# Kernel tuning notes

Hardware: AMD Instinct MI355X
Metric: run time of the kernel (lower is better)

## Reference

```python
import jax, jax.numpy as jnp
import numpy as np

D_K = 64  # d_model=512 // n_heads=8, hardcoded in source
NEG = -1e9


def setup_inputs() -> dict:
    key = jax.random.key(0)
    kq, kk, kv, km = jax.random.split(key, 4)
    B, H, S, D = 2, 8, 2048, D_K
    Q = jax.random.normal(kq, (B, H, S, D), dtype=jnp.float32)
    K = jax.random.normal(kk, (B, H, S, D), dtype=jnp.float32)
    V = jax.random.normal(kv, (B, H, S, D), dtype=jnp.float32)
    attn_mask = jax.random.randint(km, (B, H, S, S), 0, 2).astype(jnp.bool_)
    return {"Q": Q, "K": K, "V": V, "attn_mask": attn_mask}


def reference(Q, K, V, attn_mask):
    # scores = Q @ (K^T / sqrt(d_k))  -- scale applied to K^T as in source
    scale = 1.0 / np.sqrt(D_K).astype(np.float32)
    scores = jnp.einsum('bhqd,bhkd->bhqk', Q, K * scale)
    scores = jnp.where(attn_mask, NEG, scores)
    attn = jax.nn.softmax(scores, axis=-1)
    context = jnp.einsum('bhqk,bhkd->bhqd', attn, V)
    return (context, attn)
```

## Files before the change

### kernel.cpp

```cpp
#include <hip/hip_runtime.h>

typedef float f32x4 __attribute__((ext_vector_type(4)));
typedef _Float16 f16x4 __attribute__((ext_vector_type(4)));
typedef unsigned int u32x4 __attribute__((ext_vector_type(4)));
typedef __bf16 bf16x8_t __attribute__((ext_vector_type(8)));
typedef __bf16 bf16x4_t __attribute__((ext_vector_type(4)));

#define DEVFN static __device__ __forceinline__

constexpr int BHN = 16;
constexpr int SN  = 2048;
constexpr int DN  = 64;
constexpr size_t CTXN = (size_t)BHN * SN * DN;
constexpr int NK1 = 4;
constexpr int NK2 = 4;

DEVFN void qk4_mfma(f32x4& dA, f32x4& dB, bf16x8_t k0v, bf16x8_t k1v,
                    bf16x8_t qA0, bf16x8_t qA1, bf16x8_t qB0, bf16x8_t qB1) {
  asm volatile("s_nop 3\n\t"
               "v_mfma_f32_16x16x32_bf16 %0, %2, %4, %0\n\t"
               "v_mfma_f32_16x16x32_bf16 %1, %2, %6, %1\n\t"
               "v_mfma_f32_16x16x32_bf16 %0, %3, %5, %0\n\t"
               "v_mfma_f32_16x16x32_bf16 %1, %3, %7, %1\n\t"
               "s_nop 7\n\ts_nop 7"
               : "+v"(dA), "+v"(dB)
               : "v"(k0v), "v"(k1v), "v"(qA0), "v"(qA1), "v"(qB0), "v"(qB1));
}

DEVFN void pv8_mfma(f32x4& a0, f32x4& a1, f32x4& a2, f32x4& a3,
                    f32x4& b0, f32x4& b1, f32x4& b2, f32x4& b3,
                    bf16x4_t paA, bf16x4_t paB,
                    bf16x4_t v0, bf16x4_t v1, bf16x4_t v2, bf16x4_t v3) {
  asm volatile("s_nop 3\n\t"
               "v_mfma_f32_16x16x16_bf16 %0, %8, %10, %0\n\t"
               "v_mfma_f32_16x16x16_bf16 %4, %9, %10, %4\n\t"
               "v_mfma_f32_16x16x16_bf16 %1, %8, %11, %1\n\t"
               "v_mfma_f32_16x16x16_bf16 %5, %9, %11, %5\n\t"
               "v_mfma_f32_16x16x16_bf16 %2, %8, %12, %2\n\t"
               "v_mfma_f32_16x16x16_bf16 %6, %9, %12, %6\n\t"
               "v_mfma_f32_16x16x16_bf16 %3, %8, %13, %3\n\t"
               "v_mfma_f32_16x16x16_bf16 %7, %9, %13, %7\n\t"
               "s_nop 7\n\ts_nop 7"
               : "+v"(a0), "+v"(a1), "+v"(a2), "+v"(a3),
                 "+v"(b0), "+v"(b1), "+v"(b2), "+v"(b3)
               : "v"(paA), "v"(paB), "v"(v0), "v"(v1), "v"(v2), "v"(v3));
}

__global__ __launch_bounds__(256) void pack_mask_T_kernel(
    const void* __restrict__ mraw, unsigned int* __restrict__ bmT) {
  __shared__ unsigned int sfl;
  if (threadIdx.x == 0) sfl = 0;
  __syncthreads();
  {
    unsigned int f = 0;
    const unsigned int* m32 = (const unsigned int*)mraw;
    for (int i = threadIdx.x; i < 4096; i += 256) {
      unsigned int w = m32[i];
      if (w == 0x3F800000u) f |= 2u;
      else if (w > 1u) f |= 1u;
    }
    if (f) atomicOr(&sfl, f);
  }
  __syncthreads();
  const unsigned int fl = (sfl & 2u) ? 2u : ((sfl & 1u) ? 1u : 0u);

  const int tid = blockIdx.x * 256 + threadIdx.x;
  const int NT  = gridDim.x * 256;
  if (fl != 1u) {
    const int W = BHN * (SN / 32) * SN;
    const unsigned int* m32 = (const unsigned int*)mraw;
    for (int w = tid; w < W; w += NT) {
      const int q   = w & (SN - 1);
      const int kc2 = (w >> 11) & (SN / 32 - 1);
      const int bh  = w >> 17;
      const unsigned int* src = m32 + ((size_t)(bh * SN + q) * SN) + kc2 * 32;
      unsigned int r = 0;
      #pragma unroll
      for (int j = 0; j < 8; ++j) {
        u32x4 v = *(const u32x4*)(src + j * 4);
        r |= ((unsigned)(v[0] != 0u)) << (4 * j)
           | ((unsigned)(v[1] != 0u)) << (4 * j + 1)
           | ((unsigned)(v[2] != 0u)) << (4 * j + 2)
           | ((unsigned)(v[3] != 0u)) << (4 * j + 3);
      }
      bmT[w] = r;
    }
  } else {
    const int W4 = BHN * (SN / 128) * SN;
    const unsigned char* m8 = (const unsigned char*)mraw;
    for (int w4 = tid; w4 < W4; w4 += NT) {
      const int q   = w4 & (SN - 1);
      const int kc8 = (w4 >> 11) & (SN / 128 - 1);
      const int bh  = w4 >> 15;
      const unsigned char* src = m8 + ((size_t)(bh * SN + q) * SN) + kc8 * 128;
      #pragma unroll
      for (int i = 0; i < 4; ++i) {
        const unsigned int* s32 = (const unsigned int*)(src + 32 * i);
        unsigned int r = 0;
        #pragma unroll
        for (int j = 0; j < 8; ++j) {
          unsigned int x = s32[j];
          r |= ((unsigned)((x & 0x000000FFu) != 0u)) << (4 * j)
             | ((unsigned)((x & 0x0000FF00u) != 0u)) << (4 * j + 1)
             | ((unsigned)((x & 0x00FF0000u) != 0u)) << (4 * j + 2)
             | ((unsigned)((x & 0xFF000000u) != 0u)) << (4 * j + 3);
        }
        bmT[((size_t)(bh * (SN / 32) + kc8 * 4 + i)) * SN + q] = r;
      }
    }
  }
}

__global__ __launch_bounds__(256) void conv_qk_kernel(
    const float* __restrict__ Q, const float* __restrict__ K,
    __bf16* __restrict__ Qb, __bf16* __restrict__ Kb) {
  const size_t i = ((size_t)blockIdx.x * 256 + threadIdx.x) * 4;
  const float* src = blockIdx.y ? K : Q;
  __bf16* dst = blockIdx.y ? Kb : Qb;
  const float scale = blockIdx.y ? 0.125f : 1.0f;
  f32x4 v = *(const f32x4*)(src + i);
  bf16x4_t o = {(__bf16)(v[0] * scale), (__bf16)(v[1] * scale),
                (__bf16)(v[2] * scale), (__bf16)(v[3] * scale)};
  *(bf16x4_t*)(dst + i) = o;
}

__global__ __launch_bounds__(256) void conv_vt_kernel(
    const float* __restrict__ V, __bf16* __restrict__ Vt) {
  const int lane = threadIdx.x & 63, wv = threadIdx.x >> 6;
  const int k0 = (blockIdx.x * 4 + wv) * 32;
  const int bh = blockIdx.y;
  const float* src = V + (size_t)bh * SN * DN;
  __bf16* dst = Vt + (((size_t)bh * (SN / 32) + (k0 >> 5)) * DN + lane) * 32;
  bf16x8_t w0, w1, w2, w3;
  #pragma unroll
  for (int i = 0; i < 8; ++i) {
    w0[i] = (__bf16)src[(size_t)(k0 + i) * DN + lane];
    w1[i] = (__bf16)src[(size_t)(k0 + 8 + i) * DN + lane];
    w2[i] = (__bf16)src[(size_t)(k0 + 16 + i) * DN + lane];
    w3[i] = (__bf16)src[(size_t)(k0 + 24 + i) * DN + lane];
  }
  *(bf16x8_t*)(dst)      = w0;
  *(bf16x8_t*)(dst + 8)  = w1;
  *(bf16x8_t*)(dst + 16) = w2;
  *(bf16x8_t*)(dst + 24) = w3;
}

DEVFN void swz_decode(int bid, int& bh, int& c, int& x) {
  const int xcd = bid & 7, s8 = bid >> 3;
  bh = xcd + 8 * (s8 >> 6);
  const int r6 = s8 & 63;
  c = r6 >> 4;
  x = r6 & 15;
}

__global__ __launch_bounds__(256, 4) void attn_l_kernel(
    const __bf16* __restrict__ Qb, const __bf16* __restrict__ Kb,
    const unsigned int* __restrict__ bmT, float* __restrict__ lpart) {
  const int lane = threadIdx.x & 63, wv = threadIdx.x >> 6;
  const int qr = lane & 15, g = lane >> 4;
  int bh, c, x;
  swz_decode(blockIdx.x, bh, c, x);
  const int q0 = x * 128 + wv * 32;
  const int CS = SN / NK1, kbeg = c * CS;
  const __bf16* Qbb = Qb + (size_t)bh * SN * DN;
  const __bf16* Kbb = Kb + (size_t)bh * SN * DN;
  const int qA = q0 + qr, qB = q0 + 16 + qr;
  bf16x8_t qfA0 = *(const bf16x8_t*)(Qbb + (size_t)qA * DN + 8 * g);
  bf16x8_t qfA1 = *(const bf16x8_t*)(Qbb + (size_t)qA * DN + 32 + 8 * g);
  bf16x8_t qfB0 = *(const bf16x8_t*)(Qbb + (size_t)qB * DN + 8 * g);
  bf16x8_t qfB1 = *(const bf16x8_t*)(Qbb + (size_t)qB * DN + 32 + 8 * g);
  const size_t rowA = (size_t)bh * SN + qA;
  const size_t rowB = (size_t)bh * SN + qB;
  const unsigned int* bmb = bmT + (size_t)bh * (SN / 32) * SN;

  bf16x8_t kf0 = *(const bf16x8_t*)(Kbb + (size_t)(kbeg + qr) * DN + 8 * g);
  bf16x8_t kf1 = *(const bf16x8_t*)(Kbb + (size_t)(kbeg + qr) * DN + 32 + 8 * g);
  float lA = 0.f, lB = 0.f;
  unsigned int wmA = 0, wmB = 0;
  #pragma unroll 2
  for (int t = 0; t < CS / 16; ++t) {
    const int kt = kbeg + t * 16;
    const int kn = kbeg + ((t + 1) & (CS / 16 - 1)) * 16;
    bf16x8_t nk0 = *(const bf16x8_t*)(Kbb + (size_t)(kn + qr) * DN + 8 * g);
    bf16x8_t nk1 = *(const bf16x8_t*)(Kbb + (size_t)(kn + qr) * DN + 32 + 8 * g);
    if ((t & 1) == 0) {
      wmA = bmb[(size_t)(kt >> 5) * SN + qA];
      wmB = bmb[(size_t)(kt >> 5) * SN + qB];
    }
    f32x4 aA = {0,0,0,0}, aB = {0,0,0,0};
    qk4_mfma(aA, aB, kf0, kf1, qfA0, qfA1, qfB0, qfB1);
    const int sh = (kt & 16) + 4 * g;
    lA += ((wmA >> (sh + 0)) & 1u) ? 0.f : __expf(aA[0]);
    lA += ((wmA >> (sh + 1)) & 1u) ? 0.f : __expf(aA[1]);
    lA += ((wmA >> (sh + 2)) & 1u) ? 0.f : __expf(aA[2]);
    lA += ((wmA >> (sh + 3)) & 1u) ? 0.f : __expf(aA[3]);
    lB += ((wmB >> (sh + 0)) & 1u) ? 0.f : __expf(aB[0]);
    lB += ((wmB >> (sh + 1)) & 1u) ? 0.f : __expf(aB[1]);
    lB += ((wmB >> (sh + 2)) & 1u) ? 0.f : __expf(aB[2]);
    lB += ((wmB >> (sh + 3)) & 1u) ? 0.f : __expf(aB[3]);
    kf0 = nk0; kf1 = nk1;
  }
  lA = lA + __shfl_xor(lA, 16); lA = lA + __shfl_xor(lA, 32);
  lB = lB + __shfl_xor(lB, 16); lB = lB + __shfl_xor(lB, 32);
  if (g == 0) {
    lpart[rowA * NK1 + c] = lA;
    lpart[rowB * NK1 + c] = lB;
  }
}

__global__ __launch_bounds__(256, 4) void attn_out_kernel(
    const __bf16* __restrict__ Qb, const __bf16* __restrict__ Kb,
    const __bf16* __restrict__ Vt, const unsigned int* __restrict__ bmT,
    const float* __restrict__ lpart, _Float16* __restrict__ cp,
    float* __restrict__ attn) {
  __shared__ __align__(16) char Ks[2][4096];
  __shared__ __align__(16) char Vs[2][4096];
  const int tid = threadIdx.x;
  const int lane = tid & 63, wv = tid >> 6;
  const int qr = lane & 15, g = lane >> 4;
  int bh, c, x;
  swz_decode(blockIdx.x, bh, c, x);
  const int q0 = x * 128 + wv * 32;
  const int CS = SN / NK2, kbase = c * CS;
  const int NT = CS / 32;

  const __bf16* Qbb = Qb + (size_t)bh * SN * DN;
  const int qA = q0 + qr, qB = q0 + 16 + qr;
  bf16x8_t qfA0 = *(const bf16x8_t*)(Qbb + (size_t)qA * DN + 8 * g);
  bf16x8_t qfA1 = *(const bf16x8_t*)(Qbb + (size_t)qA * DN + 32 + 8 * g);
  bf16x8_t qfB0 = *(const bf16x8_t*)(Qbb + (size_t)qB * DN + 8 * g);
  bf16x8_t qfB1 = *(const bf16x8_t*)(Qbb + (size_t)qB * DN + 32 + 8 * g);
  const size_t rowA = (size_t)bh * SN + qA;
  const size_t rowB = (size_t)bh * SN + qB;
  f32x4 l4A = *(const f32x4*)(lpart + rowA * NK1);
  f32x4 l4B = *(const f32x4*)(lpart + rowB * NK1);
  const float rlA = 1.0f / (l4A[0] + l4A[1] + l4A[2] + l4A[3]);
  const float rlB = 1.0f / (l4B[0] + l4B[1] + l4B[2] + l4B[3]);
  const unsigned int* bmb = bmT + (size_t)bh * (SN / 32) * SN;
  float* arowA = attn + rowA * SN;
  float* arowB = attn + rowB * SN;

  const int krow = tid >> 3;
  const int kcolb = (tid & 7) * 16;
  const int kdst = krow * 128 + (kcolb ^ ((krow & 7) << 4));
  const char* Ksrc = (const char*)(Kb + (size_t)bh * SN * DN + (size_t)kbase * DN);
  const int vd = tid >> 2;
  const int vkb = (tid & 3) * 16;
  const int vdst0 = vd * 64 + ((vkb    ) ^ ((vd & 7) << 3));
  const int vdst1 = vd * 64 + ((vkb + 8) ^ ((vd & 7) << 3));
  const char* Vsrc = (const char*)Vt + ((size_t)bh * (SN / 32) + (kbase >> 5)) * 4096;

  f32x4 cA0 = {0,0,0,0}, cA1 = {0,0,0,0}, cA2 = {0,0,0,0}, cA3 = {0,0,0,0};
  f32x4 cB0 = {0,0,0,0}, cB1 = {0,0,0,0}, cB2 = {0,0,0,0}, cB3 = {0,0,0,0};

  {
    u32x4 kr = *(const u32x4*)(Ksrc + krow * 128 + kcolb);
    u32x4 vr = *(const u32x4*)(Vsrc + tid * 16);
    *(u32x4*)&Ks[0][kdst] = kr;
    *(unsigned long long*)&Vs[0][vdst0] =
        ((unsigned long long)vr[1] << 32) | vr[0];
    *(unsigned long long*)&Vs[0][vdst1] =
        ((unsigned long long)vr[3] << 32) | vr[2];
  }
  __syncthreads();

  for (int tt = 0; tt < NT; ++tt) {
    const bool pf = (tt + 1 < NT);
    u32x4 kr, vr;
    if (pf) {
      kr = *(const u32x4*)(Ksrc + (tt + 1) * 4096 + krow * 128 + kcolb);
      vr = *(const u32x4*)(Vsrc + (tt + 1) * 4096 + tid * 16);
    }
    const char* Kbuf = Ks[tt & 1];
    const char* Vbuf = Vs[tt & 1];
    const int ktg = kbase + tt * 32;
    const unsigned int wmA = bmb[(size_t)((kbase >> 5) + tt) * SN + qA];
    const unsigned int wmB = bmb[(size_t)((kbase >> 5) + tt) * SN + qB];
    #pragma unroll
    for (int s = 0; s < 2; ++s) {
      const int rk = 16 * s + qr;
      bf16x8_t kf0 = *(const bf16x8_t*)&Kbuf[rk * 128 + ((16 * g     ) ^ ((rk & 7) << 4))];
      bf16x8_t kf1 = *(const bf16x8_t*)&Kbuf[rk * 128 + ((64 + 16 * g) ^ ((rk & 7) << 4))];
      const int vxor = (32 * s + 8 * g) ^ ((qr & 7) << 3);
      bf16x4_t vf0 = *(const bf16x4_t*)&Vbuf[(qr     ) * 64 + vxor];
      bf16x4_t vf1 = *(const bf16x4_t*)&Vbuf[(qr + 16) * 64 + vxor];
      bf16x4_t vf2 = *(const bf16x4_t*)&Vbuf[(qr + 32) * 64 + vxor];
      bf16x4_t vf3 = *(const bf16x4_t*)&Vbuf[(qr + 48) * 64 + vxor];
      f32x4 aA = {0,0,0,0}, aB = {0,0,0,0};
      qk4_mfma(aA, aB, kf0, kf1, qfA0, qfA1, qfB0, qfB1);
      const int sh = 16 * s + 4 * g;
      float pA0 = (((wmA >> (sh + 0)) & 1u) ? 0.f : __expf(aA[0])) * rlA;
      float pA1 = (((wmA >> (sh + 1)) & 1u) ? 0.f : __expf(aA[1])) * rlA;
      float pA2 = (((wmA >> (sh + 2)) & 1u) ? 0.f : __expf(aA[2])) * rlA;
      float pA3 = (((wmA >> (sh + 3)) & 1u) ? 0.f : __expf(aA[3])) * rlA;
      float pB0 = (((wmB >> (sh + 0)) & 1u) ? 0.f : __expf(aB[0])) * rlB;
      float pB1 = (((wmB >> (sh + 1)) & 1u) ? 0.f : __expf(aB[1])) * rlB;
      float pB2 = (((wmB >> (sh + 2)) & 1u) ? 0.f : __expf(aB[2])) * rlB;
      float pB3 = (((wmB >> (sh + 3)) & 1u) ? 0.f : __expf(aB[3])) * rlB;
      *(f32x4*)(arowA + ktg + sh) = (f32x4){pA0, pA1, pA2, pA3};
      *(f32x4*)(arowB + ktg + sh) = (f32x4){pB0, pB1, pB2, pB3};
      bf16x4_t paA = {(__bf16)pA0, (__bf16)pA1, (__bf16)pA2, (__bf16)pA3};
      bf16x4_t paB = {(__bf16)pB0, (__bf16)pB1, (__bf16)pB2, (__bf16)pB3};
      pv8_mfma(cA0, cA1, cA2, cA3, cB0, cB1, cB2, cB3, paA, paB, vf0, vf1, vf2, vf3);
    }
    if (pf) {
      char* Kn = Ks[(tt + 1) & 1];
      char* Vn = Vs[(tt + 1) & 1];
      *(u32x4*)&Kn[kdst] = kr;
      *(unsigned long long*)&Vn[vdst0] = ((unsigned long long)vr[1] << 32) | vr[0];
      *(unsigned long long*)&Vn[vdst1] = ((unsigned long long)vr[3] << 32) | vr[2];
    }
    __syncthreads();
  }
  _Float16* cdst = cp + (size_t)c * CTXN;
  const size_t baseo = (size_t)bh * SN * DN;
  #pragma unroll
  for (int j = 0; j < 4; ++j) {
    const size_t rA = baseo + (size_t)(q0 + 4 * g + j) * DN + qr;
    const size_t rB = baseo + (size_t)(q0 + 16 + 4 * g + j) * DN + qr;
    cdst[rA]      = (_Float16)cA0[j];
    cdst[rA + 16] = (_Float16)cA1[j];
    cdst[rA + 32] = (_Float16)cA2[j];
    cdst[rA + 48] = (_Float16)cA3[j];
    cdst[rB]      = (_Float16)cB0[j];
    cdst[rB + 16] = (_Float16)cB1[j];
    cdst[rB + 32] = (_Float16)cB2[j];
    cdst[rB + 48] = (_Float16)cB3[j];
  }
}

__global__ __launch_bounds__(256) void ctx_reduce_kernel(
    const _Float16* __restrict__ cp, float* __restrict__ ctx) {
  const size_t i = ((size_t)blockIdx.x * 256 + threadIdx.x) * 4;
  f16x4 a = *(const f16x4*)(cp + i);
  f16x4 b = *(const f16x4*)(cp + CTXN + i);
  f16x4 d = *(const f16x4*)(cp + 2 * CTXN + i);
  f16x4 e = *(const f16x4*)(cp + 3 * CTXN + i);
  f32x4 s;
  #pragma unroll
  for (int k = 0; k < 4; ++k)
    s[k] = ((float)a[k] + (float)b[k]) + ((float)d[k] + (float)e[k]);
  __builtin_nontemporal_store(s, (f32x4*)(ctx + i));
}

extern "C" void kernel_launch(void* const* d_in, const int* in_sizes, int n_in,
                              void* d_out, int out_size, void* d_ws, size_t ws_size,
                              hipStream_t stream) {
  const float* Q = (const float*)d_in[0];
  const float* K = (const float*)d_in[1];
  const float* V = (const float*)d_in[2];
  const void*  mraw = d_in[3];

  float* out  = (float*)d_out;
  float* ctx  = out;
  float* attn = out + CTXN;

  char* wsb = (char*)d_ws;
  unsigned int* bmT = (unsigned int*)(wsb + 256);
  float* lp   = (float*)(wsb + 256 + 8388608);
  __bf16* Qb  = (__bf16*)(wsb + 256 + 8388608 + 524288);
  __bf16* Kb  = (__bf16*)(wsb + 256 + 8388608 + 524288 + 4194304);
  __bf16* Vt  = (__bf16*)(wsb + 256 + 8388608 + 524288 + 2 * 4194304);
  _Float16* cp = (_Float16*)(wsb + 256 + 8388608 + 524288 + 3 * 4194304);

  pack_mask_T_kernel<<<2048, 256, 0, stream>>>(mraw, bmT);
  conv_qk_kernel<<<dim3(2048, 2), 256, 0, stream>>>(Q, K, Qb, Kb);
  conv_vt_kernel<<<dim3(16, BHN), 256, 0, stream>>>(V, Vt);

  attn_l_kernel<<<1024, 256, 0, stream>>>(Qb, Kb, bmT, lp);
  attn_out_kernel<<<1024, 256, 0, stream>>>(Qb, Kb, Vt, bmT, lp, cp, attn);
  ctx_reduce_kernel<<<2048, 256, 0, stream>>>(cp, ctx);
}
```

Before: 232.8 us.

## Merge prep kernels into one launch and stage K tiles through LDS in attn_l

The three preprocessing kernels (mask bit-pack, Q/K bf16 conversion, V transpose) are combined into a single launch that dispatches on block index, and the Q/K conversion now handles 8 elements per thread. attn_l_kernel now loads 64-row K tiles cooperatively into double-buffered, XOR-swizzled shared memory, with a register prefetch of the next tile, instead of having each wave read K directly from global memory. This aims to cut launch overhead and redundant global K traffic across the four waves. In exchange it adds a block barrier per tile and uses more LDS, which may lower occupancy.

```diff
diff --git a/kernel.cpp b/kernel.cpp
--- a/kernel.cpp
+++ b/kernel.cpp
@@ -46,103 +46,111 @@
                : "v"(paA), "v"(paB), "v"(v0), "v"(v1), "v"(v2), "v"(v3));
 }
 
-__global__ __launch_bounds__(256) void pack_mask_T_kernel(
-    const void* __restrict__ mraw, unsigned int* __restrict__ bmT) {
-  __shared__ unsigned int sfl;
-  if (threadIdx.x == 0) sfl = 0;
-  __syncthreads();
-  {
-    unsigned int f = 0;
-    const unsigned int* m32 = (const unsigned int*)mraw;
-    for (int i = threadIdx.x; i < 4096; i += 256) {
-      unsigned int w = m32[i];
-      if (w == 0x3F800000u) f |= 2u;
-      else if (w > 1u) f |= 1u;
-    }
-    if (f) atomicOr(&sfl, f);
-  }
-  __syncthreads();
-  const unsigned int fl = (sfl & 2u) ? 2u : ((sfl & 1u) ? 1u : 0u);
-
-  const int tid = blockIdx.x * 256 + threadIdx.x;
-  const int NT  = gridDim.x * 256;
-  if (fl != 1u) {
-    const int W = BHN * (SN / 32) * SN;
-    const unsigned int* m32 = (const unsigned int*)mraw;
-    for (int w = tid; w < W; w += NT) {
-      const int q   = w & (SN - 1);
-      const int kc2 = (w >> 11) & (SN / 32 - 1);
-      const int bh  = w >> 17;
-      const unsigned int* src = m32 + ((size_t)(bh * SN + q) * SN) + kc2 * 32;
-      unsigned int r = 0;
-      #pragma unroll
-      for (int j = 0; j < 8; ++j) {
-        u32x4 v = *(const u32x4*)(src + j * 4);
-        r |= ((unsigned)(v[0] != 0u)) << (4 * j)
-           | ((unsigned)(v[1] != 0u)) << (4 * j + 1)
-           | ((unsigned)(v[2] != 0u)) << (4 * j + 2)
-           | ((unsigned)(v[3] != 0u)) << (4 * j + 3);
+constexpr int PB = 2048, QB = 1024, KB = 1024, VB = 256;
+
+__global__ __launch_bounds__(256) void prep_kernel(
+    const void* __restrict__ mraw, unsigned int* __restrict__ bmT,
+    const float* __restrict__ Q, const float* __restrict__ K,
+    const float* __restrict__ V, __bf16* __restrict__ Qb,
+    __bf16* __restrict__ Kb, __bf16* __restrict__ Vt) {
+  const int bid = blockIdx.x;
+  const int tidl = threadIdx.x;
+  if (bid < PB) {
+    __shared__ unsigned int sfl;
+    if (tidl == 0) sfl = 0;
+    __syncthreads();
+    {
+      unsigned int f = 0;
+      const unsigned int* m32 = (const unsigned int*)mraw;
+      for (int i = tidl; i < 4096; i += 256) {
+        unsigned int w = m32[i];
+        if (w == 0x3F800000u) f |= 2u;
+        else if (w > 1u) f |= 1u;
       }
-      bmT[w] = r;
-    }
-  } else {
-    const int W4 = BHN * (SN / 128) * SN;
-    const unsigned char* m8 = (const unsigned char*)mraw;
-    for (int w4 = tid; w4 < W4; w4 += NT) {
-      const int q   = w4 & (SN - 1);
-      const int kc8 = (w4 >> 11) & (SN / 128 - 1);
-      const int bh  = w4 >> 15;
-      const unsigned char* src = m8 + ((size_t)(bh * SN + q) * SN) + kc8 * 128;
-      #pragma unroll
-      for (int i = 0; i < 4; ++i) {
-        const unsigned int* s32 = (const unsigned int*)(src + 32 * i);
+      if (f) atomicOr(&sfl, f);
+    }
+    __syncthreads();
+    const unsigned int fl = (sfl & 2u) ? 2u : ((sfl & 1u) ? 1u : 0u);
+    const int tid = bid * 256 + tidl;
+    const int NT  = PB * 256;
+    if (fl != 1u) {
+      const int W = BHN * (SN / 32) * SN;
+      const unsigned int* m32 = (const unsigned int*)mraw;
+      for (int w = tid; w < W; w += NT) {
+        const int q   = w & (SN - 1);
+        const int kc2 = (w >> 11) & (SN / 32 - 1);
+        const int bh  = w >> 17;
+        const unsigned int* src = m32 + ((size_t)(bh * SN + q) * SN) + kc2 * 32;
         unsigned int r = 0;
         #pragma unroll
         for (int j = 0; j < 8; ++j) {
-          unsigned int x = s32[j];
-          r |= ((unsigned)((x & 0x000000FFu) != 0u)) << (4 * j)
-             | ((unsigned)((x & 0x0000FF00u) != 0u)) << (4 * j + 1)
-             | ((unsigned)((x & 0x00FF0000u) != 0u)) << (4 * j + 2)
-             | ((unsigned)((x & 0xFF000000u) != 0u)) << (4 * j + 3);
+          u32x4 v = *(const u32x4*)(src + j * 4);
+          r |= ((unsigned)(v[0] != 0u)) << (4 * j)
+             | ((unsigned)(v[1] != 0u)) << (4 * j + 1)
+             | ((unsigned)(v[2] != 0u)) << (4 * j + 2)
+             | ((unsigned)(v[3] != 0u)) << (4 * j + 3);
         }
-        bmT[((size_t)(bh * (SN / 32) + kc8 * 4 + i)) * SN + q] = r;
+        bmT[w] = r;
       }
-    }
-  }
-}
-
-__global__ __launch_bounds__(256) void conv_qk_kernel(
-    const float* __restrict__ Q, const float* __restrict__ K,
-    __bf16* __restrict__ Qb, __bf16* __restrict__ Kb) {
-  const size_t i = ((size_t)blockIdx.x * 256 + threadIdx.x) * 4;
-  const float* src = blockIdx.y ? K : Q;
-  __bf16* dst = blockIdx.y ? Kb : Qb;
-  const float scale = blockIdx.y ? 0.125f : 1.0f;
-  f32x4 v = *(const f32x4*)(src + i);
-  bf16x4_t o = {(__bf16)(v[0] * scale), (__bf16)(v[1] * scale),
-                (__bf16)(v[2] * scale), (__bf16)(v[3] * scale)};
-  *(bf16x4_t*)(dst + i) = o;
-}
-
-__global__ __launch_bounds__(256) void conv_vt_kernel(
-    const float* __restrict__ V, __bf16* __restrict__ Vt) {
-  const int lane = threadIdx.x & 63, wv = threadIdx.x >> 6;
-  const int k0 = (blockIdx.x * 4 + wv) * 32;
-  const int bh = blockIdx.y;
-  const float* src = V + (size_t)bh * SN * DN;
-  __bf16* dst = Vt + (((size_t)bh * (SN / 32) + (k0 >> 5)) * DN + lane) * 32;
-  bf16x8_t w0, w1, w2, w3;
-  #pragma unroll
-  for (int i = 0; i < 8; ++i) {
-    w0[i] = (__bf16)src[(size_t)(k0 + i) * DN + lane];
-    w1[i] = (__bf16)src[(size_t)(k0 + 8 + i) * DN + lane];
-    w2[i] = (__bf16)src[(size_t)(k0 + 16 + i) * DN + lane];
-    w3[i] = (__bf16)src[(size_t)(k0 + 24 + i) * DN + lane];
-  }
-  *(bf16x8_t*)(dst)      = w0;
-  *(bf16x8_t*)(dst + 8)  = w1;
-  *(bf16x8_t*)(dst + 16) = w2;
-  *(bf16x8_t*)(dst + 24) = w3;
+    } else {
+      const int W4 = BHN * (SN / 128) * SN;
+      const unsigned char* m8 = (const unsigned char*)mraw;
+      for (int w4 = tid; w4 < W4; w4 += NT) {
+        const int q   = w4 & (SN - 1);
+        const int kc8 = (w4 >> 11) & (SN / 128 - 1);
+        const int bh  = w4 >> 15;
+        const unsigned char* src = m8 + ((size_t)(bh * SN + q) * SN) + kc8 * 128;
+        #pragma unroll
+        for (int i = 0; i < 4; ++i) {
+          const unsigned int* s32 = (const unsigned int*)(src + 32 * i);
+          unsigned int r = 0;
+          #pragma unroll
+          for (int j = 0; j < 8; ++j) {
+            unsigned int x = s32[j];
+            r |= ((unsigned)((x & 0x000000FFu) != 0u)) << (4 * j)
+               | ((unsigned)((x & 0x0000FF00u) != 0u)) << (4 * j + 1)
+               | ((unsigned)((x & 0x00FF0000u) != 0u)) << (4 * j + 2)
+               | ((unsigned)((x & 0xFF000000u) != 0u)) << (4 * j + 3);
+          }
+          bmT[((size_t)(bh * (SN / 32) + kc8 * 4 + i)) * SN + q] = r;
+        }
+      }
+    }
+  } else if (bid < PB + QB + KB) {
+    const bool isK = (bid >= PB + QB);
+    const int rb = bid - (isK ? PB + QB : PB);
+    const float* src = isK ? K : Q;
+    __bf16* dst = isK ? Kb : Qb;
+    const float scale = isK ? 0.125f : 1.0f;
+    const size_t i = ((size_t)rb * 256 + tidl) * 8;
+    f32x4 v0 = *(const f32x4*)(src + i);
+    f32x4 v1 = *(const f32x4*)(src + i + 4);
+    bf16x8_t o;
+    o[0]=(__bf16)(v0[0]*scale); o[1]=(__bf16)(v0[1]*scale);
+    o[2]=(__bf16)(v0[2]*scale); o[3]=(__bf16)(v0[3]*scale);
+    o[4]=(__bf16)(v1[0]*scale); o[5]=(__bf16)(v1[1]*scale);
+    o[6]=(__bf16)(v1[2]*scale); o[7]=(__bf16)(v1[3]*scale);
+    *(bf16x8_t*)(dst + i) = o;
+  } else {
+    const int vb = bid - (PB + QB + KB);
+    const int lane = tidl & 63, wv = tidl >> 6;
+    const int k0 = ((vb & 15) * 4 + wv) * 32;
+    const int bh = vb >> 4;
+    const float* src = V + (size_t)bh * SN * DN;
+    __bf16* dst = Vt + (((size_t)bh * (SN / 32) + (k0 >> 5)) * DN + lane) * 32;
+    bf16x8_t w0, w1, w2, w3;
+    #pragma unroll
+    for (int i = 0; i < 8; ++i) {
+      w0[i] = (__bf16)src[(size_t)(k0 + i) * DN + lane];
+      w1[i] = (__bf16)src[(size_t)(k0 + 8 + i) * DN + lane];
+      w2[i] = (__bf16)src[(size_t)(k0 + 16 + i) * DN + lane];
+      w3[i] = (__bf16)src[(size_t)(k0 + 24 + i) * DN + lane];
+    }
+    *(bf16x8_t*)(dst)      = w0;
+    *(bf16x8_t*)(dst + 8)  = w1;
+    *(bf16x8_t*)(dst + 16) = w2;
+    *(bf16x8_t*)(dst + 24) = w3;
+  }
 }
 
 DEVFN void swz_decode(int bid, int& bh, int& c, int& x) {
@@ -156,14 +164,17 @@
 __global__ __launch_bounds__(256, 4) void attn_l_kernel(
     const __bf16* __restrict__ Qb, const __bf16* __restrict__ Kb,
     const unsigned int* __restrict__ bmT, float* __restrict__ lpart) {
-  const int lane = threadIdx.x & 63, wv = threadIdx.x >> 6;
+  __shared__ __align__(16) char Ks[2][8192];
+  const int tid = threadIdx.x;
+  const int lane = tid & 63, wv = tid >> 6;
   const int qr = lane & 15, g = lane >> 4;
   int bh, c, x;
   swz_decode(blockIdx.x, bh, c, x);
   const int q0 = x * 128 + wv * 32;
-  const int CS = SN / NK1, kbeg = c * CS;
+  const int CS = SN / NK1, kbase = c * CS;
+  const int NT = CS / 64;
+
   const __bf16* Qbb = Qb + (size_t)bh * SN * DN;
-  const __bf16* Kbb = Kb + (size_t)bh * SN * DN;
   const int qA = q0 + qr, qB = q0 + 16 + qr;
   bf16x8_t qfA0 = *(const bf16x8_t*)(Qbb + (size_t)qA * DN + 8 * g);
   bf16x8_t qfA1 = *(const bf16x8_t*)(Qbb + (size_t)qA * DN + 32 + 8 * g);
@@ -172,33 +183,62 @@
   const size_t rowA = (size_t)bh * SN + qA;
   const size_t rowB = (size_t)bh * SN + qB;
   const unsigned int* bmb = bmT + (size_t)bh * (SN / 32) * SN;
-
-  bf16x8_t kf0 = *(const bf16x8_t*)(Kbb + (size_t)(kbeg + qr) * DN + 8 * g);
-  bf16x8_t kf1 = *(const bf16x8_t*)(Kbb + (size_t)(kbeg + qr) * DN + 32 + 8 * g);
+  const int kb2 = kbase >> 5;
+
+  const int krow = tid >> 2;
+  const int kcol = (tid & 3) * 32;
+  const int swz  = (krow & 7) << 4;
+  const int kdst0 = krow * 128 + ((kcol     ) ^ swz);
+  const int kdst1 = krow * 128 + ((kcol + 16) ^ swz);
+  const char* Ksrc = (const char*)(Kb + (size_t)bh * SN * DN + (size_t)kbase * DN);
+
+  {
+    u32x4 a = *(const u32x4*)(Ksrc + krow * 128 + kcol);
+    u32x4 b = *(const u32x4*)(Ksrc + krow * 128 + kcol + 16);
+    *(u32x4*)&Ks[0][kdst0] = a;
+    *(u32x4*)&Ks[0][kdst1] = b;
+  }
+  __syncthreads();
+
   float lA = 0.f, lB = 0.f;
-  unsigned int wmA = 0, wmB = 0;
-  #pragma unroll 2
-  for (int t = 0; t < CS / 16; ++t) {
-    const int kt = kbeg + t * 16;
-    const int kn = kbeg + ((t + 1) & (CS / 16 - 1)) * 16;
-    bf16x8_t nk0 = *(const bf16x8_t*)(Kbb + (size_t)(kn + qr) * DN + 8 * g);
-    bf16x8_t nk1 = *(const bf16x8_t*)(Kbb + (size_t)(kn + qr) * DN + 32 + 8 * g);
-    if ((t & 1) == 0) {
-      wmA = bmb[(size_t)(kt >> 5) * SN + qA];
-      wmB = bmb[(size_t)(kt >> 5) * SN + qB];
-    }
-    f32x4 aA = {0,0,0,0}, aB = {0,0,0,0};
-    qk4_mfma(aA, aB, kf0, kf1, qfA0, qfA1, qfB0, qfB1);
-    const int sh = (kt & 16) + 4 * g;
-    lA += ((wmA >> (sh + 0)) & 1u) ? 0.f : __expf(aA[0]);
-    lA += ((wmA >> (sh + 1)) & 1u) ? 0.f : __expf(aA[1]);
-    lA += ((wmA >> (sh + 2)) & 1u) ? 0.f : __expf(aA[2]);
-    lA += ((wmA >> (sh + 3)) & 1u) ? 0.f : __expf(aA[3]);
-    lB += ((wmB >> (sh + 0)) & 1u) ? 0.f : __expf(aB[0]);
-    lB += ((wmB >> (sh + 1)) & 1u) ? 0.f : __expf(aB[1]);
-    lB += ((wmB >> (sh + 2)) & 1u) ? 0.f : __expf(aB[2]);
-    lB += ((wmB >> (sh + 3)) & 1u) ? 0.f : __expf(aB[3]);
-    kf0 = nk0; kf1 = nk1;
+  for (int tt = 0; tt < NT; ++tt) {
+    const bool pf = (tt + 1 < NT);
+    u32x4 a, b;
+    if (pf) {
+      a = *(const u32x4*)(Ksrc + (tt + 1) * 8192 + krow * 128 + kcol);
+      b = *(const u32x4*)(Ksrc + (tt + 1) * 8192 + krow * 128 + kcol + 16);
+    }
+    const char* Kbuf = Ks[tt & 1];
+    const unsigned int wA0 = bmb[(size_t)(kb2 + 2 * tt    ) * SN + qA];
+    const unsigned int wA1 = bmb[(size_t)(kb2 + 2 * tt + 1) * SN + qA];
+    const unsigned int wB0 = bmb[(size_t)(kb2 + 2 * tt    ) * SN + qB];
+    const unsigned int wB1 = bmb[(size_t)(kb2 + 2 * tt + 1) * SN + qB];
+    #pragma unroll
+    for (int s = 0; s < 4; ++s) {
+      const int rk = 16 * s + qr;
+      const int rsw = (rk & 7) << 4;
+      bf16x8_t kf0 = *(const bf16x8_t*)&Kbuf[rk * 128 + ((16 * g     ) ^ rsw)];
+      bf16x8_t kf1 = *(const bf16x8_t*)&Kbuf[rk * 128 + ((64 + 16 * g) ^ rsw)];
+      f32x4 aA = {0,0,0,0}, aB = {0,0,0,0};
+      qk4_mfma(aA, aB, kf0, kf1, qfA0, qfA1, qfB0, qfB1);
+      const unsigned int wmA = (s < 2) ? wA0 : wA1;
+      const unsigned int wmB = (s < 2) ? wB0 : wB1;
+      const int sh = (s & 1) * 16 + 4 * g;
+      lA += ((wmA >> (sh + 0)) & 1u) ? 0.f : __expf(aA[0]);
+      lA += ((wmA >> (sh + 1)) & 1u) ? 0.f : __expf(aA[1]);
+      lA += ((wmA >> (sh + 2)) & 1u) ? 0.f : __expf(aA[2]);
+      lA += ((wmA >> (sh + 3)) & 1u) ? 0.f : __expf(aA[3]);
+      lB += ((wmB >> (sh + 0)) & 1u) ? 0.f : __expf(aB[0]);
+      lB += ((wmB >> (sh + 1)) & 1u) ? 0.f : __expf(aB[1]);
+      lB += ((wmB >> (sh + 2)) & 1u) ? 0.f : __expf(aB[2]);
+      lB += ((wmB >> (sh + 3)) & 1u) ? 0.f : __expf(aB[3]);
+    }
+    if (pf) {
+      char* Kn = Ks[(tt + 1) & 1];
+      *(u32x4*)&Kn[kdst0] = a;
+      *(u32x4*)&Kn[kdst1] = b;
+    }
+    __syncthreads();
   }
   lA = lA + __shfl_xor(lA, 16); lA = lA + __shfl_xor(lA, 32);
   lB = lB + __shfl_xor(lB, 16); lB = lB + __shfl_xor(lB, 32);
@@ -363,10 +403,7 @@
   __bf16* Vt  = (__bf16*)(wsb + 256 + 8388608 + 524288 + 2 * 4194304);
   _Float16* cp = (_Float16*)(wsb + 256 + 8388608 + 524288 + 3 * 4194304);
 
-  pack_mask_T_kernel<<<2048, 256, 0, stream>>>(mraw, bmT);
-  conv_qk_kernel<<<dim3(2048, 2), 256, 0, stream>>>(Q, K, Qb, Kb);
-  conv_vt_kernel<<<dim3(16, BHN), 256, 0, stream>>>(V, Vt);
-
+  prep_kernel<<<PB + QB + KB + VB, 256, 0, stream>>>(mraw, bmT, Q, K, V, Qb, Kb, Vt);
   attn_l_kernel<<<1024, 256, 0, stream>>>(Qb, Kb, bmT, lp);
   attn_out_kernel<<<1024, 256, 0, stream>>>(Qb, Kb, Vt, bmT, lp, cp, attn);
   ctx_reduce_kernel<<<2048, 256, 0, stream>>>(cp, ctx);
```

Result: faster. 202.5 us (median of 2 runs) (-13.0%).
